# Kernel tuning notes

Hardware: AMD Instinct MI355X
Metric: run time of the kernel (lower is better)

The kernel has to match this reference:

```python
import jax, jax.numpy as jnp
import numpy as np

VOCAB = 50000
DIM = 128
B = 1024
LQ = 32
LD = 512
KERNEL_NUM = 21
SIGMA = 0.1
EXACT_SIGMA = 0.001
OUT_LAYERS = [10, 5]
EPS = 1e-12  # F.normalize eps


def _kernel_params():
    step = 2.0 / (KERNEL_NUM - 1)
    mus = (np.arange(-1.0, 1.0, step) + step / 2).astype(np.float32)  # 20 soft bins
    mus = np.concatenate([mus, np.array([1.0], dtype=np.float32)])   # exact-match bin
    sigmas = np.array([SIGMA] * (KERNEL_NUM - 1) + [EXACT_SIGMA], dtype=np.float32)
    return mus, sigmas


def _normalize(x):
    n = jnp.linalg.norm(x, axis=-1, keepdims=True)
    return x / jnp.maximum(n, EPS)


def _predict(emb, w0, b0, w1, b1, w2, b2, q, d):
    eq = _normalize(emb[q])  # [B, Lq, D]
    ed = _normalize(emb[d])  # [B, Ld, D]
    mm = jnp.einsum('bld,brd->blr', eq, ed)  # cosine matching matrix [B, Lq, Ld]
    mus, sigmas = _kernel_params()
    feats = [
        jnp.log1p(jnp.exp(-(mm - mu) ** 2 / (2.0 * sig * sig)).sum(-1)).sum(-1)
        for mu, sig in zip(mus, sigmas)
    ]
    x = jnp.stack(feats, axis=1)  # [B, KERNEL_NUM]
    h = jax.nn.relu(x @ w0.T + b0)
    h = jax.nn.relu(h @ w1.T + b1)
    return h @ w2.T + b2  # [B, 1]


def setup_inputs() -> dict:
    key = jax.random.key(0)
    ks = jax.random.split(key, 12)
    emb = jax.random.normal(ks[0], (VOCAB, DIM), jnp.float32) * 0.1
    emb = emb.at[0].set(0.0)  # padding_idx=0 row
    q1 = jax.random.randint(ks[1], (B, LQ), 0, VOCAB)
    d1 = jax.random.randint(ks[2], (B, LD), 0, VOCAB)
    q2 = jax.random.randint(ks[3], (B, LQ), 0, VOCAB)
    d2 = jax.random.randint(ks[4], (B, LD), 0, VOCAB)
    dims = [KERNEL_NUM] + OUT_LAYERS + [1]
    def lin(k, fan_in, fan_out):
        bound = 1.0 / np.sqrt(fan_in)
        kw, kb = jax.random.split(k)
        w = jax.random.uniform(kw, (fan_out, fan_in), jnp.float32, -bound, bound)
        b = jax.random.uniform(kb, (fan_out,), jnp.float32, -bound, bound)
        return w, b
    w0, b0 = lin(ks[5], dims[0], dims[1])
    w1, b1 = lin(ks[6], dims[1], dims[2])
    w2, b2 = lin(ks[7], dims[2], dims[3])
    return dict(emb=emb, w0=w0, b0=b0, w1=w1, b1=b1, w2=w2, b2=b2,
                query_1=q1, document_1=d1, query_2=q2, document_2=d2)


def reference(emb, w0, b0, w1, b1, w2, b2, query_1, document_1, query_2, document_2):
    logits_1 = _predict(emb, w0, b0, w1, b1, w2, b2, query_1, document_1)
    logits_2 = _predict(emb, w0, b0, w1, b1, w2, b2, query_2, document_2)
    return jax.nn.sigmoid(logits_1 - logits_2)
```

## Files before the change

### kernel.cpp

```cpp
#include <hip/hip_runtime.h>
#include <hip/hip_bf16.h>
#include <math.h>

#define LQ    32
#define LD    512
#define DIM   128
#define NK    21
#define VOCAB 50000

typedef __attribute__((ext_vector_type(8))) short short8;
typedef __attribute__((ext_vector_type(4))) float f32x4;
typedef __attribute__((ext_vector_type(2))) float f32x2;

__device__ __forceinline__ unsigned pkbf(float a, float b) {
    unsigned short ua = __bfloat16_as_ushort(__float2bfloat16(a));
    unsigned short ub = __bfloat16_as_ushort(__float2bfloat16(b));
    return (unsigned)ua | ((unsigned)ub << 16);
}

__global__ __launch_bounds__(256, 8)
void knrm_prep(const float* __restrict__ emb, unsigned* __restrict__ emb16) {
    int row  = blockIdx.x * 4 + (threadIdx.x >> 6);
    int lane = threadIdx.x & 63;
    if (row >= VOCAB) return;
    float2 v = ((const float2*)(emb + (size_t)row * DIM))[lane];
    float ss = v.x * v.x + v.y * v.y;
    #pragma unroll
    for (int s = 1; s < 64; s <<= 1) ss += __shfl_xor(ss, s, 64);
    float rn = 1.0f / fmaxf(sqrtf(ss), 1e-12f);
    emb16[(size_t)row * 64 + lane] = pkbf(v.x * rn, v.y * rn);
}

__global__ __launch_bounds__(256, 4)
void knrm_main(const unsigned short* __restrict__ emb16,
               const float* __restrict__ w0, const float* __restrict__ b0,
               const float* __restrict__ w1, const float* __restrict__ b1,
               const float* __restrict__ w2, const float* __restrict__ b2,
               const int* __restrict__ q1, const int* __restrict__ d1,
               const int* __restrict__ q2, const int* __restrict__ d2,
               float* __restrict__ out)
{
    __shared__ __align__(16) char smem[16016];
    unsigned short (*Bq)[DIM] = (unsigned short(*)[DIM])(smem);
    float (*SSh)[LQ][20] = (float(*)[LQ][20])(smem);
    int*   dtok0 = (int*)(smem + 10240);
    float (*SSe)[LQ] = (float(*)[LQ])(smem + 12288);
    int*   qtok0 = (int*)(smem + 13312);
    float* xw    = (float*)(smem + 13440);
    float* h0s   = (float*)(smem + 13776);
    float* h1s   = (float*)(smem + 13816);
    int*   dtok1 = (int*)(smem + 13840);
    int*   qtok1 = (int*)(smem + 15888);

    const int b    = blockIdx.x;
    const int tid  = threadIdx.x;
    const int w    = tid >> 6;
    const int lane = tid & 63;
    const int rg   = lane >> 4;
    const int l15  = lane & 15;

    if (tid < LQ) {
        qtok0[tid] = q1[b * LQ + tid];
        qtok1[tid] = q2[b * LQ + tid];
    }
    dtok0[tid]       = d1[b * LD + tid];
    dtok0[tid + 256] = d1[b * LD + tid + 256];
    dtok1[tid]       = d2[b * LD + tid];
    dtok1[tid + 256] = d2[b * LD + tid + 256];
    __syncthreads();

    float lg0 = 0.0f;

    #pragma unroll 1
    for (int side = 0; side < 2; ++side) {
        const int* qts = side ? qtok1 : qtok0;
        const int* dts = side ? dtok1 : dtok0;

        #pragma unroll
        for (int cc = 0; cc < 2; ++cc) {
            int rloc = cc * 4 + rg;
            int tok  = qts[w * 8 + rloc];
            int sw   = (rloc & 7) << 3;
            int col  = (l15 * 8) ^ sw;
            const unsigned short* src = emb16 + (size_t)tok * DIM + col;
            __builtin_amdgcn_global_load_lds(src, &Bq[w * 8 + cc * 4][0], 16, 0, 0);
        }

        {
            int q = tid & 31, g = tid >> 5;
            int qv = qts[q];
            int c = 0;
            const int4* dp = (const int4*)&dts[g * 64];
            #pragma unroll
            for (int j = 0; j < 16; ++j) {
                int4 dv = dp[j];
                c += (dv.x == qv) + (dv.y == qv) + (dv.z == qv) + (dv.w == qv);
            }
            SSe[g][q] = (qv == 0) ? 0.0f : (float)c;
        }
        __syncthreads();

        const int dbase = w * 128;
        int tok0 = dts[dbase + l15];
        const unsigned short* ap0 = emb16 + (size_t)tok0 * DIM + rg * 8;
        short8 a0 = *(const short8*)(ap0);
        short8 a1 = *(const short8*)(ap0 + 32);
        short8 a2 = *(const short8*)(ap0 + 64);
        short8 a3 = *(const short8*)(ap0 + 96);

        const int swB = (l15 & 7) << 3;
        short8 bq0[4], bq1[4];
        #pragma unroll
        for (int g = 0; g < 4; ++g) {
            bq0[g] = *(const short8*)&Bq[l15][(g * 32 + rg * 8) ^ swB];
            bq1[g] = *(const short8*)&Bq[l15 + 16][(g * 32 + rg * 8) ^ swB];
        }
        __syncthreads();

        f32x2 accP[10], accM[10];
        #pragma unroll
        for (int j = 0; j < 10; ++j) {
            accP[j] = (f32x2){0.0f, 0.0f};
            accM[j] = (f32x2){0.0f, 0.0f};
        }

        auto chain2 = [&](f32x2 x) {
            f32x2 t1 = x * -72.134752f + 7.2134752f;
            f32x2 Ea = t1 * x + -0.18033688f;
            f32x2 Ra = x * 14.4269504f + -0.7213475f;
            f32x2 E, R, rc;
            E.x = __builtin_amdgcn_exp2f(Ea.x);
            E.y = __builtin_amdgcn_exp2f(Ea.y);
            R.x = __builtin_amdgcn_exp2f(Ra.x);
            R.y = __builtin_amdgcn_exp2f(Ra.y);
            rc.x = __builtin_amdgcn_rcpf(R.x);
            rc.y = __builtin_amdgcn_rcpf(R.y);
            f32x2 tP = E;
            f32x2 tM = E * rc;
            accP[0] += tP; accM[0] += tM;
            #pragma unroll
            for (int j = 1; j < 10; ++j) {
                tP *= R; tM *= rc;
                accP[j] += tP; accM[j] += tM;
            }
        };

        auto mfma8 = [&](f32x4& c0, f32x4& c1) {
            c0 = __builtin_amdgcn_mfma_f32_16x16x32_bf16(a0, bq0[0], c0, 0, 0, 0);
            c1 = __builtin_amdgcn_mfma_f32_16x16x32_bf16(a0, bq1[0], c1, 0, 0, 0);
            c0 = __builtin_amdgcn_mfma_f32_16x16x32_bf16(a1, bq0[1], c0, 0, 0, 0);
            c1 = __builtin_amdgcn_mfma_f32_16x16x32_bf16(a1, bq1[1], c1, 0, 0, 0);
            c0 = __builtin_amdgcn_mfma_f32_16x16x32_bf16(a2, bq0[2], c0, 0, 0, 0);
            c1 = __builtin_amdgcn_mfma_f32_16x16x32_bf16(a2, bq1[2], c1, 0, 0, 0);
            c0 = __builtin_amdgcn_mfma_f32_16x16x32_bf16(a3, bq0[3], c0, 0, 0, 0);
            c1 = __builtin_amdgcn_mfma_f32_16x16x32_bf16(a3, bq1[3], c1, 0, 0, 0);
        };

        #pragma unroll 1
        for (int t = 0; t < 7; ++t) {
            f32x4 c0 = {0, 0, 0, 0}, c1 = {0, 0, 0, 0};
            mfma8(c0, c1);

            int ntok = dts[dbase + (t + 1) * 16 + l15];
            const unsigned short* np = emb16 + (size_t)ntok * DIM + rg * 8;
            short8 n0 = *(const short8*)(np);
            short8 n1 = *(const short8*)(np + 32);
            short8 n2 = *(const short8*)(np + 64);
            short8 n3 = *(const short8*)(np + 96);

            #pragma unroll
            for (int r = 0; r < 4; ++r) {
                f32x2 x; x.x = c0[r]; x.y = c1[r];
                chain2(x);
            }
            a0 = n0; a1 = n1; a2 = n2; a3 = n3;
        }
        {
            f32x4 c0 = {0, 0, 0, 0}, c1 = {0, 0, 0, 0};
            mfma8(c0, c1);
            #pragma unroll
            for (int r = 0; r < 4; ++r) {
                f32x2 x; x.x = c0[r]; x.y = c1[r];
                chain2(x);
            }
        }

        #pragma unroll
        for (int j = 0; j < 10; ++j) {
            accP[j].x += __shfl_xor(accP[j].x, 16, 64); accP[j].x += __shfl_xor(accP[j].x, 32, 64);
            accP[j].y += __shfl_xor(accP[j].y, 16, 64); accP[j].y += __shfl_xor(accP[j].y, 32, 64);
            accM[j].x += __shfl_xor(accM[j].x, 16, 64); accM[j].x += __shfl_xor(accM[j].x, 32, 64);
            accM[j].y += __shfl_xor(accM[j].y, 16, 64); accM[j].y += __shfl_xor(accM[j].y, 32, 64);
        }
        if (lane < 16) {
            const float GP[10] = {1.0f, 0.60653066f, 0.13533528f, 0.011108997f,
                                  3.3546263e-4f, 3.7266532e-6f, 1.5229979e-8f,
                                  2.2897348e-11f, 1.2664166e-14f, 2.5767430e-18f};
            const float GM[10] = {0.60653066f, 0.13533528f, 0.011108997f,
                                  3.3546263e-4f, 3.7266532e-6f, 1.5229979e-8f,
                                  2.2897348e-11f, 1.2664166e-14f, 2.5767430e-18f,
                                  1.9287498e-22f};
            #pragma unroll
            for (int j = 0; j < 10; ++j) {
                SSh[w][l15][10 + j]      = accP[j].x * GP[j];
                SSh[w][l15][9 - j]       = accM[j].x * GM[j];
                SSh[w][l15 + 16][10 + j] = accP[j].y * GP[j];
                SSh[w][l15 + 16][9 - j]  = accM[j].y * GM[j];
            }
        }
        __syncthreads();

        if (lane < NK) {
            float s = 0.0f;
            #pragma unroll
            for (int qq = 0; qq < 8; ++qq) {
                int q = w * 8 + qq;
                float v;
                if (lane == 20) {
                    v = SSe[0][q] + SSe[1][q] + SSe[2][q] + SSe[3][q]
                      + SSe[4][q] + SSe[5][q] + SSe[6][q] + SSe[7][q];
                } else {
                    v = SSh[0][q][lane] + SSh[1][q][lane]
                      + SSh[2][q][lane] + SSh[3][q][lane];
                }
                s += log1pf(v);
            }
            xw[w * NK + lane] = s;
        }
        __syncthreads();

        if (tid < 10) {
            float s = b0[tid];
            #pragma unroll
            for (int k = 0; k < NK; ++k) {
                float xv = xw[k] + xw[NK + k] + xw[2 * NK + k] + xw[3 * NK + k];
                s = fmaf(xv, w0[tid * NK + k], s);
            }
            h0s[tid] = fmaxf(s, 0.0f);
        }
        __syncthreads();
        if (tid < 5) {
            float s = b1[tid];
            #pragma unroll
            for (int k = 0; k < 10; ++k) s = fmaf(h0s[k], w1[tid * 10 + k], s);
            h1s[tid] = fmaxf(s, 0.0f);
        }
        __syncthreads();
        if (tid == 0) {
            float s = b2[0];
            #pragma unroll
            for (int k = 0; k < 5; ++k) s = fmaf(h1s[k], w2[k], s);
            if (side == 0) lg0 = s;
            else out[b] = 1.0f / (1.0f + __expf(-(lg0 - s)));
        }
    }
}

extern "C" void kernel_launch(void* const* d_in, const int* in_sizes, int n_in,
                              void* d_out, int out_size, void* d_ws, size_t ws_size,
                              hipStream_t stream) {
    const float* emb = (const float*)d_in[0];
    const float* w0  = (const float*)d_in[1];
    const float* b0  = (const float*)d_in[2];
    const float* w1  = (const float*)d_in[3];
    const float* b1  = (const float*)d_in[4];
    const float* w2  = (const float*)d_in[5];
    const float* b2  = (const float*)d_in[6];
    const int*   q1  = (const int*)d_in[7];
    const int*   d1  = (const int*)d_in[8];
    const int*   q2  = (const int*)d_in[9];
    const int*   d2  = (const int*)d_in[10];
    float* out = (float*)d_out;

    unsigned* emb16 = (unsigned*)d_ws;

    knrm_prep<<<(VOCAB + 3) / 4, 256, 0, stream>>>(emb, emb16);
    knrm_main<<<1024, 256, 0, stream>>>((const unsigned short*)emb16,
                                        w0, b0, w1, b1, w2, b2,
                                        q1, d1, q2, d2, out);
}
```

Measured before the change: 82.07 us.

## Split query/document sides into separate blocks and finalize sigmoid in new kernel

Each block now handles only one of the two sides for a batch element, so the main kernel launches 2048 blocks instead of 1024 running two sides in sequence. Per-side logits go to workspace, and a small third kernel takes their difference and applies the sigmoid. This doubles the grid to improve occupancy and latency hiding across the GPU, and shrinks shared memory per block. The cost is an extra kernel launch and a round trip through global memory for the logits.

```diff
diff --git a/kernel.cpp b/kernel.cpp
--- a/kernel.cpp
+++ b/kernel.cpp
@@ -38,221 +38,220 @@
                const float* __restrict__ w2, const float* __restrict__ b2,
                const int* __restrict__ q1, const int* __restrict__ d1,
                const int* __restrict__ q2, const int* __restrict__ d2,
-               float* __restrict__ out)
+               float* __restrict__ logits)
 {
-    __shared__ __align__(16) char smem[16016];
+    __shared__ __align__(16) char smem[14176];
     unsigned short (*Bq)[DIM] = (unsigned short(*)[DIM])(smem);
     float (*SSh)[LQ][20] = (float(*)[LQ][20])(smem);
-    int*   dtok0 = (int*)(smem + 10240);
+    int*   dtokS = (int*)(smem + 10240);
     float (*SSe)[LQ] = (float(*)[LQ])(smem + 12288);
-    int*   qtok0 = (int*)(smem + 13312);
+    int*   qtokS = (int*)(smem + 13312);
     float* xw    = (float*)(smem + 13440);
     float* h0s   = (float*)(smem + 13776);
     float* h1s   = (float*)(smem + 13816);
-    int*   dtok1 = (int*)(smem + 13840);
-    int*   qtok1 = (int*)(smem + 15888);
-
-    const int b    = blockIdx.x;
+
+    const int bid  = blockIdx.x;
+    const int b    = bid >> 1;
+    const int side = bid & 1;
     const int tid  = threadIdx.x;
     const int w    = tid >> 6;
     const int lane = tid & 63;
     const int rg   = lane >> 4;
     const int l15  = lane & 15;
 
-    if (tid < LQ) {
-        qtok0[tid] = q1[b * LQ + tid];
-        qtok1[tid] = q2[b * LQ + tid];
-    }
-    dtok0[tid]       = d1[b * LD + tid];
-    dtok0[tid + 256] = d1[b * LD + tid + 256];
-    dtok1[tid]       = d2[b * LD + tid];
-    dtok1[tid + 256] = d2[b * LD + tid + 256];
-    __syncthreads();
-
-    float lg0 = 0.0f;
-
-    #pragma unroll 1
-    for (int side = 0; side < 2; ++side) {
-        const int* qts = side ? qtok1 : qtok0;
-        const int* dts = side ? dtok1 : dtok0;
-
+    const int* qt = (side ? q2 : q1) + b * LQ;
+    const int* dt = (side ? d2 : d1) + b * LD;
+
+    if (tid < LQ) qtokS[tid] = qt[tid];
+    dtokS[tid]       = dt[tid];
+    dtokS[tid + 256] = dt[tid + 256];
+    __syncthreads();
+
+    {
         #pragma unroll
         for (int cc = 0; cc < 2; ++cc) {
             int rloc = cc * 4 + rg;
-            int tok  = qts[w * 8 + rloc];
+            int tok  = qtokS[w * 8 + rloc];
             int sw   = (rloc & 7) << 3;
             int col  = (l15 * 8) ^ sw;
             const unsigned short* src = emb16 + (size_t)tok * DIM + col;
             __builtin_amdgcn_global_load_lds(src, &Bq[w * 8 + cc * 4][0], 16, 0, 0);
         }
-
-        {
-            int q = tid & 31, g = tid >> 5;
-            int qv = qts[q];
-            int c = 0;
-            const int4* dp = (const int4*)&dts[g * 64];
-            #pragma unroll
-            for (int j = 0; j < 16; ++j) {
-                int4 dv = dp[j];
-                c += (dv.x == qv) + (dv.y == qv) + (dv.z == qv) + (dv.w == qv);
+    }
+
+    {
+        int q = tid & 31, g = tid >> 5;
+        int qv = qtokS[q];
+        int c = 0;
+        const int4* dp = (const int4*)&dtokS[g * 64];
+        #pragma unroll
+        for (int j = 0; j < 16; ++j) {
+            int4 dv = dp[j];
+            c += (dv.x == qv) + (dv.y == qv) + (dv.z == qv) + (dv.w == qv);
+        }
+        SSe[g][q] = (qv == 0) ? 0.0f : (float)c;
+    }
+    __syncthreads();
+
+    const int dbase = w * 128;
+    int tok0 = dtokS[dbase + l15];
+    const unsigned short* ap0 = emb16 + (size_t)tok0 * DIM + rg * 8;
+    short8 a0 = *(const short8*)(ap0);
+    short8 a1 = *(const short8*)(ap0 + 32);
+    short8 a2 = *(const short8*)(ap0 + 64);
+    short8 a3 = *(const short8*)(ap0 + 96);
+
+    const int swB = (l15 & 7) << 3;
+    short8 bq0[4], bq1[4];
+    #pragma unroll
+    for (int g = 0; g < 4; ++g) {
+        bq0[g] = *(const short8*)&Bq[l15][(g * 32 + rg * 8) ^ swB];
+        bq1[g] = *(const short8*)&Bq[l15 + 16][(g * 32 + rg * 8) ^ swB];
+    }
+    __syncthreads();
+
+    f32x2 accP[10], accM[10];
+    #pragma unroll
+    for (int j = 0; j < 10; ++j) {
+        accP[j] = (f32x2){0.0f, 0.0f};
+        accM[j] = (f32x2){0.0f, 0.0f};
+    }
+
+    auto chain2 = [&](f32x2 x) {
+        f32x2 t1 = x * -72.134752f + 7.2134752f;
+        f32x2 Ea = t1 * x + -0.18033688f;
+        f32x2 Ra = x * 14.4269504f + -0.7213475f;
+        f32x2 E, R, rc;
+        E.x = __builtin_amdgcn_exp2f(Ea.x);
+        E.y = __builtin_amdgcn_exp2f(Ea.y);
+        R.x = __builtin_amdgcn_exp2f(Ra.x);
+        R.y = __builtin_amdgcn_exp2f(Ra.y);
+        rc.x = __builtin_amdgcn_rcpf(R.x);
+        rc.y = __builtin_amdgcn_rcpf(R.y);
+        f32x2 tP = E;
+        f32x2 tM = E * rc;
+        accP[0] += tP; accM[0] += tM;
+        #pragma unroll
+        for (int j = 1; j < 10; ++j) {
+            tP *= R; tM *= rc;
+            accP[j] += tP; accM[j] += tM;
+        }
+    };
+
+    auto mfma8 = [&](f32x4& c0, f32x4& c1) {
+        c0 = __builtin_amdgcn_mfma_f32_16x16x32_bf16(a0, bq0[0], c0, 0, 0, 0);
+        c1 = __builtin_amdgcn_mfma_f32_16x16x32_bf16(a0, bq1[0], c1, 0, 0, 0);
+        c0 = __builtin_amdgcn_mfma_f32_16x16x32_bf16(a1, bq0[1], c0, 0, 0, 0);
+        c1 = __builtin_amdgcn_mfma_f32_16x16x32_bf16(a1, bq1[1], c1, 0, 0, 0);
+        c0 = __builtin_amdgcn_mfma_f32_16x16x32_bf16(a2, bq0[2], c0, 0, 0, 0);
+        c1 = __builtin_amdgcn_mfma_f32_16x16x32_bf16(a2, bq1[2], c1, 0, 0, 0);
+        c0 = __builtin_amdgcn_mfma_f32_16x16x32_bf16(a3, bq0[3], c0, 0, 0, 0);
+        c1 = __builtin_amdgcn_mfma_f32_16x16x32_bf16(a3, bq1[3], c1, 0, 0, 0);
+    };
+
+    #pragma unroll 1
+    for (int t = 0; t < 7; ++t) {
+        f32x4 c0 = {0, 0, 0, 0}, c1 = {0, 0, 0, 0};
+        mfma8(c0, c1);
+
+        int ntok = dtokS[dbase + (t + 1) * 16 + l15];
+        const unsigned short* np = emb16 + (size_t)ntok * DIM + rg * 8;
+        short8 n0 = *(const short8*)(np);
+        short8 n1 = *(const short8*)(np + 32);
+        short8 n2 = *(const short8*)(np + 64);
+        short8 n3 = *(const short8*)(np + 96);
+
+        #pragma unroll
+        for (int r = 0; r < 4; ++r) {
+            f32x2 x; x.x = c0[r]; x.y = c1[r];
+            chain2(x);
+        }
+        a0 = n0; a1 = n1; a2 = n2; a3 = n3;
+    }
+    {
+        f32x4 c0 = {0, 0, 0, 0}, c1 = {0, 0, 0, 0};
+        mfma8(c0, c1);
+        #pragma unroll
+        for (int r = 0; r < 4; ++r) {
+            f32x2 x; x.x = c0[r]; x.y = c1[r];
+            chain2(x);
+        }
+    }
+
+    #pragma unroll
+    for (int j = 0; j < 10; ++j) {
+        accP[j].x += __shfl_xor(accP[j].x, 16, 64); accP[j].x += __shfl_xor(accP[j].x, 32, 64);
+        accP[j].y += __shfl_xor(accP[j].y, 16, 64); accP[j].y += __shfl_xor(accP[j].y, 32, 64);
+        accM[j].x += __shfl_xor(accM[j].x, 16, 64); accM[j].x += __shfl_xor(accM[j].x, 32, 64);
+        accM[j].y += __shfl_xor(accM[j].y, 16, 64); accM[j].y += __shfl_xor(accM[j].y, 32, 64);
+    }
+    if (lane < 16) {
+        const float GP[10] = {1.0f, 0.60653066f, 0.13533528f, 0.011108997f,
+                              3.3546263e-4f, 3.7266532e-6f, 1.5229979e-8f,
+                              2.2897348e-11f, 1.2664166e-14f, 2.5767430e-18f};
+        const float GM[10] = {0.60653066f, 0.13533528f, 0.011108997f,
+                              3.3546263e-4f, 3.7266532e-6f, 1.5229979e-8f,
+                              2.2897348e-11f, 1.2664166e-14f, 2.5767430e-18f,
+                              1.9287498e-22f};
+        #pragma unroll
+        for (int j = 0; j < 10; ++j) {
+            SSh[w][l15][10 + j]      = accP[j].x * GP[j];
+            SSh[w][l15][9 - j]       = accM[j].x * GM[j];
+            SSh[w][l15 + 16][10 + j] = accP[j].y * GP[j];
+            SSh[w][l15 + 16][9 - j]  = accM[j].y * GM[j];
+        }
+    }
+    __syncthreads();
+
+    if (lane < NK) {
+        float s = 0.0f;
+        #pragma unroll
+        for (int qq = 0; qq < 8; ++qq) {
+            int q = w * 8 + qq;
+            float v;
+            if (lane == 20) {
+                v = SSe[0][q] + SSe[1][q] + SSe[2][q] + SSe[3][q]
+                  + SSe[4][q] + SSe[5][q] + SSe[6][q] + SSe[7][q];
+            } else {
+                v = SSh[0][q][lane] + SSh[1][q][lane]
+                  + SSh[2][q][lane] + SSh[3][q][lane];
             }
-            SSe[g][q] = (qv == 0) ? 0.0f : (float)c;
-        }
-        __syncthreads();
-
-        const int dbase = w * 128;
-        int tok0 = dts[dbase + l15];
-        const unsigned short* ap0 = emb16 + (size_t)tok0 * DIM + rg * 8;
-        short8 a0 = *(const short8*)(ap0);
-        short8 a1 = *(const short8*)(ap0 + 32);
-        short8 a2 = *(const short8*)(ap0 + 64);
-        short8 a3 = *(const short8*)(ap0 + 96);
-
-        const int swB = (l15 & 7) << 3;
-        short8 bq0[4], bq1[4];
-        #pragma unroll
-        for (int g = 0; g < 4; ++g) {
-            bq0[g] = *(const short8*)&Bq[l15][(g * 32 + rg * 8) ^ swB];
-            bq1[g] = *(const short8*)&Bq[l15 + 16][(g * 32 + rg * 8) ^ swB];
-        }
-        __syncthreads();
-
-        f32x2 accP[10], accM[10];
-        #pragma unroll
-        for (int j = 0; j < 10; ++j) {
-            accP[j] = (f32x2){0.0f, 0.0f};
-            accM[j] = (f32x2){0.0f, 0.0f};
-        }
-
-        auto chain2 = [&](f32x2 x) {
-            f32x2 t1 = x * -72.134752f + 7.2134752f;
-            f32x2 Ea = t1 * x + -0.18033688f;
-            f32x2 Ra = x * 14.4269504f + -0.7213475f;
-            f32x2 E, R, rc;
-            E.x = __builtin_amdgcn_exp2f(Ea.x);
-            E.y = __builtin_amdgcn_exp2f(Ea.y);
-            R.x = __builtin_amdgcn_exp2f(Ra.x);
-            R.y = __builtin_amdgcn_exp2f(Ra.y);
-            rc.x = __builtin_amdgcn_rcpf(R.x);
-            rc.y = __builtin_amdgcn_rcpf(R.y);
-            f32x2 tP = E;
-            f32x2 tM = E * rc;
-            accP[0] += tP; accM[0] += tM;
-            #pragma unroll
-            for (int j = 1; j < 10; ++j) {
-                tP *= R; tM *= rc;
-                accP[j] += tP; accM[j] += tM;
-            }
-        };
-
-        auto mfma8 = [&](f32x4& c0, f32x4& c1) {
-            c0 = __builtin_amdgcn_mfma_f32_16x16x32_bf16(a0, bq0[0], c0, 0, 0, 0);
-            c1 = __builtin_amdgcn_mfma_f32_16x16x32_bf16(a0, bq1[0], c1, 0, 0, 0);
-            c0 = __builtin_amdgcn_mfma_f32_16x16x32_bf16(a1, bq0[1], c0, 0, 0, 0);
-            c1 = __builtin_amdgcn_mfma_f32_16x16x32_bf16(a1, bq1[1], c1, 0, 0, 0);
-            c0 = __builtin_amdgcn_mfma_f32_16x16x32_bf16(a2, bq0[2], c0, 0, 0, 0);
-            c1 = __builtin_amdgcn_mfma_f32_16x16x32_bf16(a2, bq1[2], c1, 0, 0, 0);
-            c0 = __builtin_amdgcn_mfma_f32_16x16x32_bf16(a3, bq0[3], c0, 0, 0, 0);
-            c1 = __builtin_amdgcn_mfma_f32_16x16x32_bf16(a3, bq1[3], c1, 0, 0, 0);
-        };
-
-        #pragma unroll 1
-        for (int t = 0; t < 7; ++t) {
-            f32x4 c0 = {0, 0, 0, 0}, c1 = {0, 0, 0, 0};
-            mfma8(c0, c1);
-
-            int ntok = dts[dbase + (t + 1) * 16 + l15];
-            const unsigned short* np = emb16 + (size_t)ntok * DIM + rg * 8;
-            short8 n0 = *(const short8*)(np);
-            short8 n1 = *(const short8*)(np + 32);
-            short8 n2 = *(const short8*)(np + 64);
-            short8 n3 = *(const short8*)(np + 96);
-
-            #pragma unroll
-            for (int r = 0; r < 4; ++r) {
-                f32x2 x; x.x = c0[r]; x.y = c1[r];
-                chain2(x);
-            }
-            a0 = n0; a1 = n1; a2 = n2; a3 = n3;
-        }
-        {
-            f32x4 c0 = {0, 0, 0, 0}, c1 = {0, 0, 0, 0};
-            mfma8(c0, c1);
-            #pragma unroll
-            for (int r = 0; r < 4; ++r) {
-                f32x2 x; x.x = c0[r]; x.y = c1[r];
-                chain2(x);
-            }
-        }
-
-        #pragma unroll
-        for (int j = 0; j < 10; ++j) {
-            accP[j].x += __shfl_xor(accP[j].x, 16, 64); accP[j].x += __shfl_xor(accP[j].x, 32, 64);
-            accP[j].y += __shfl_xor(accP[j].y, 16, 64); accP[j].y += __shfl_xor(accP[j].y, 32, 64);
-            accM[j].x += __shfl_xor(accM[j].x, 16, 64); accM[j].x += __shfl_xor(accM[j].x, 32, 64);
-            accM[j].y += __shfl_xor(accM[j].y, 16, 64); accM[j].y += __shfl_xor(accM[j].y, 32, 64);
-        }
-        if (lane < 16) {
-            const float GP[10] = {1.0f, 0.60653066f, 0.13533528f, 0.011108997f,
-                                  3.3546263e-4f, 3.7266532e-6f, 1.5229979e-8f,
-                                  2.2897348e-11f, 1.2664166e-14f, 2.5767430e-18f};
-            const float GM[10] = {0.60653066f, 0.13533528f, 0.011108997f,
-                                  3.3546263e-4f, 3.7266532e-6f, 1.5229979e-8f,
-                                  2.2897348e-11f, 1.2664166e-14f, 2.5767430e-18f,
-                                  1.9287498e-22f};
-            #pragma unroll
-            for (int j = 0; j < 10; ++j) {
-                SSh[w][l15][10 + j]      = accP[j].x * GP[j];
-                SSh[w][l15][9 - j]       = accM[j].x * GM[j];
-                SSh[w][l15 + 16][10 + j] = accP[j].y * GP[j];
-                SSh[w][l15 + 16][9 - j]  = accM[j].y * GM[j];
-            }
-        }
-        __syncthreads();
-
-        if (lane < NK) {
-            float s = 0.0f;
-            #pragma unroll
-            for (int qq = 0; qq < 8; ++qq) {
-                int q = w * 8 + qq;
-                float v;
-                if (lane == 20) {
-                    v = SSe[0][q] + SSe[1][q] + SSe[2][q] + SSe[3][q]
-                      + SSe[4][q] + SSe[5][q] + SSe[6][q] + SSe[7][q];
-                } else {
-                    v = SSh[0][q][lane] + SSh[1][q][lane]
-                      + SSh[2][q][lane] + SSh[3][q][lane];
-                }
-                s += log1pf(v);
-            }
-            xw[w * NK + lane] = s;
-        }
-        __syncthreads();
-
-        if (tid < 10) {
-            float s = b0[tid];
-            #pragma unroll
-            for (int k = 0; k < NK; ++k) {
-                float xv = xw[k] + xw[NK + k] + xw[2 * NK + k] + xw[3 * NK + k];
-                s = fmaf(xv, w0[tid * NK + k], s);
-            }
-            h0s[tid] = fmaxf(s, 0.0f);
-        }
-        __syncthreads();
-        if (tid < 5) {
-            float s = b1[tid];
-            #pragma unroll
-            for (int k = 0; k < 10; ++k) s = fmaf(h0s[k], w1[tid * 10 + k], s);
-            h1s[tid] = fmaxf(s, 0.0f);
-        }
-        __syncthreads();
-        if (tid == 0) {
-            float s = b2[0];
-            #pragma unroll
-            for (int k = 0; k < 5; ++k) s = fmaf(h1s[k], w2[k], s);
-            if (side == 0) lg0 = s;
-            else out[b] = 1.0f / (1.0f + __expf(-(lg0 - s)));
-        }
+            s += log1pf(v);
+        }
+        xw[w * NK + lane] = s;
+    }
+    __syncthreads();
+
+    if (tid < 10) {
+        float s = b0[tid];
+        #pragma unroll
+        for (int k = 0; k < NK; ++k) {
+            float xv = xw[k] + xw[NK + k] + xw[2 * NK + k] + xw[3 * NK + k];
+            s = fmaf(xv, w0[tid * NK + k], s);
+        }
+        h0s[tid] = fmaxf(s, 0.0f);
+    }
+    __syncthreads();
+    if (tid < 5) {
+        float s = b1[tid];
+        #pragma unroll
+        for (int k = 0; k < 10; ++k) s = fmaf(h0s[k], w1[tid * 10 + k], s);
+        h1s[tid] = fmaxf(s, 0.0f);
+    }
+    __syncthreads();
+    if (tid == 0) {
+        float s = b2[0];
+        #pragma unroll
+        for (int k = 0; k < 5; ++k) s = fmaf(h1s[k], w2[k], s);
+        logits[bid] = s;
+    }
+}
+
+__global__ void knrm_fin(const float* __restrict__ lg, float* __restrict__ out) {
+    int i = blockIdx.x * 256 + threadIdx.x;
+    if (i < 1024) {
+        float z = lg[2 * i] - lg[2 * i + 1];
+        out[i] = 1.0f / (1.0f + __expf(-z));
     }
 }
 
@@ -273,9 +272,11 @@
     float* out = (float*)d_out;
 
     unsigned* emb16 = (unsigned*)d_ws;
+    float* logits   = (float*)((char*)d_ws + 12800000);
 
     knrm_prep<<<(VOCAB + 3) / 4, 256, 0, stream>>>(emb, emb16);
-    knrm_main<<<1024, 256, 0, stream>>>((const unsigned short*)emb16,
+    knrm_main<<<2048, 256, 0, stream>>>((const unsigned short*)emb16,
                                         w0, b0, w1, b1, w2, b2,
-                                        q1, d1, q2, d2, out);
-}
+                                        q1, d1, q2, d2, logits);
+    knrm_fin<<<4, 256, 0, stream>>>(logits, out);
+}
```

After: 69.92 us. -14.8%, faster.
